# Optimization experiments

Measured on AMD Instinct MI355X. Metric: run time of the kernel, lower is better.

## Reference

```python
import jax, jax.numpy as jnp
import numpy as np

B, S, I, H, A = 512, 256, 12, 256, 9


def _lstm_layer(x, w_ih, w_hh, b_ih, b_hh):
    # x: [B,S,in] -> outputs [B,S,H], final (h, c). PyTorch gate order i,f,g,o.
    b, s, _ = x.shape
    h_dim = w_hh.shape[1]
    xg = jnp.einsum('bsi,gi->bsg', x, w_ih) + b_ih  # [B,S,4H] precomputed input gates

    def step(carry, xg_t):
        h, c = carry
        gates = xg_t + h @ w_hh.T + b_hh
        i_g, f_g, g_g, o_g = jnp.split(gates, 4, axis=-1)
        c = jax.nn.sigmoid(f_g) * c + jax.nn.sigmoid(i_g) * jnp.tanh(g_g)
        h = jax.nn.sigmoid(o_g) * jnp.tanh(c)
        return (h, c), h

    init = (jnp.zeros((b, h_dim), x.dtype), jnp.zeros((b, h_dim), x.dtype))
    (h, c), ys = jax.lax.scan(step, init, jnp.swapaxes(xg, 0, 1))
    return jnp.swapaxes(ys, 0, 1), h, c


def setup_inputs() -> dict:
    key = jax.random.key(0)
    ks = jax.random.split(key, 20)
    sc = 0.1
    inp = {
        'x': jax.random.normal(ks[0], (B, S, I), jnp.float32),
        'mask': jnp.ones((B, A), jnp.float32),
        'W_emb': jax.random.normal(ks[1], (H, I), jnp.float32) * sc,
        'b_emb': jnp.zeros((H,), jnp.float32),
        'w_ih0': jax.random.normal(ks[2], (4 * H, H), jnp.float32) * sc,
        'w_hh0': jax.random.normal(ks[3], (4 * H, H), jnp.float32) * sc,
        'b_ih0': jnp.zeros((4 * H,), jnp.float32),
        'b_hh0': jnp.zeros((4 * H,), jnp.float32),
        'w_ih1': jax.random.normal(ks[4], (4 * H, H), jnp.float32) * sc,
        'w_hh1': jax.random.normal(ks[5], (4 * H, H), jnp.float32) * sc,
        'b_ih1': jnp.zeros((4 * H,), jnp.float32),
        'b_hh1': jnp.zeros((4 * H,), jnp.float32),
        'ln_g': jnp.ones((H,), jnp.float32),
        'ln_b': jnp.zeros((H,), jnp.float32),
        'w1': jax.random.normal(ks[6], (32, H), jnp.float32) * sc,
        'b1': jnp.zeros((32,), jnp.float32),
        'w2': jax.random.normal(ks[7], (A, 32), jnp.float32) * sc,
        'b2': jnp.zeros((A,), jnp.float32),
    }
    return inp


def reference(x, mask, W_emb, b_emb, w_ih0, w_hh0, b_ih0, b_hh0,
              w_ih1, w_hh1, b_ih1, b_hh1, ln_g, ln_b, w1, b1, w2, b2):
    # embed + ReLU
    emb = jax.nn.relu(jnp.einsum('bsi,hi->bsh', x, W_emb) + b_emb)  # [B,S,H]
    # 2-layer LSTM (dropout between layers is identity in eval mode)
    y0, h0, c0 = _lstm_layer(emb, w_ih0, w_hh0, b_ih0, b_hh0)
    y1, h1, c1 = _lstm_layer(y0, w_ih1, w_hh1, b_ih1, b_hh1)
    last = y1[:, -1, :]  # [B,H]
    # LayerNorm
    mu = jnp.mean(last, axis=-1, keepdims=True)
    var = jnp.mean((last - mu) ** 2, axis=-1, keepdims=True)
    normed = (last - mu) / jnp.sqrt(var + 1e-5) * ln_g + ln_b
    # MLP head (dropout identity in eval)
    hdn = jax.nn.relu(normed @ w1.T + b1)
    logits = hdn @ w2.T + b2  # [B,A]
    logits = logits + (1.0 - mask) * -1e9
    hidden = (jnp.stack([h0, h1]), jnp.stack([c0, c1]))
    return logits, hidden
```

## Files before the change

### kernel.cpp

```cpp
#include <hip/hip_runtime.h>
#include <cstdint>
#include <cstddef>

typedef __attribute__((ext_vector_type(8))) short short8;
typedef __attribute__((ext_vector_type(4))) float f32x4;

#define MFMA16(a, b, c) __builtin_amdgcn_mfma_f32_16x16x32_bf16((a), (b), (c), 0, 0, 0)

constexpr int kB = 512, kS = 256, kI = 12, kH = 256, kA = 9;
constexpr int kNS = 8;
constexpr int kNB = 32;
constexpr int LDH = 264;
constexpr int LDG = 132;
constexpr int kBH = kB * kH;

constexpr int OUT_H = kB * kA;
constexpr int OUT_C = OUT_H + 2 * kB * kH;

__device__ __forceinline__ short f2bf(float f) {
  uint32_t u = __float_as_uint(f);
  u += 0x7fffu + ((u >> 16) & 1u);
  return (short)(u >> 16);
}
__device__ __forceinline__ float fast_sigmoid(float v) {
  return __builtin_amdgcn_rcpf(1.f + __expf(-v));
}
__device__ __forceinline__ float fast_tanh(float v) {
  return 2.f * __builtin_amdgcn_rcpf(1.f + __expf(-2.f * v)) - 1.f;
}

__global__ __launch_bounds__(256, 1) void lstm_scan_kernel(
    const float* __restrict__ x,
    const float* __restrict__ W_emb, const float* __restrict__ b_emb,
    const float* __restrict__ w_ih0, const float* __restrict__ w_hh0,
    const float* __restrict__ b_ih0, const float* __restrict__ b_hh0,
    const float* __restrict__ w_ih1, const float* __restrict__ w_hh1,
    const float* __restrict__ b_ih1, const float* __restrict__ b_hh1,
    unsigned short* __restrict__ h0ex, unsigned short* __restrict__ h1ex,
    int* __restrict__ flags0, int* __restrict__ flags1,
    float* __restrict__ dout)
{
  const int tid   = threadIdx.x;
  const int btile = blockIdx.x & (kNB - 1);
  const int slice = blockIdx.x >> 5;
  const int b0    = btile * 16;
  const int lane  = tid & 63;
  const int wave  = tid >> 6;
  const int n16   = lane & 15;
  const int quad  = lane >> 4;

  __shared__ short xlds[16 * 32];
  __shared__ short embL[16 * LDH];
  __shared__ short hA[16 * LDH];
  __shared__ short hB[16 * LDH];
  __shared__ float gL[16 * LDG];

  for (int i = tid; i < 16 * 32; i += 256) xlds[i] = 0;
  for (int i = tid; i < 16 * LDH; i += 256) { hA[i] = 0; hB[i] = 0; }

  const float* Wm[4] = { w_ih0, w_hh0, w_ih1, w_hh1 };
  short8 wB[2][4][8];
#pragma unroll
  for (int ti = 0; ti < 2; ++ti) {
    const int nt   = wave + ti * 4;
    const int gcol = (nt >> 1) * kH + slice * 32 + (nt & 1) * 16 + n16;
#pragma unroll
    for (int mat = 0; mat < 4; ++mat) {
      const float* wp = Wm[mat] + (size_t)gcol * kH;
#pragma unroll
      for (int kk = 0; kk < 8; ++kk) {
        const float* p = wp + kk * 32 + quad * 8;
        const float4 f0 = *(const float4*)p;
        const float4 f1 = *(const float4*)(p + 4);
        short8 v;
        v[0] = f2bf(f0.x); v[1] = f2bf(f0.y); v[2] = f2bf(f0.z); v[3] = f2bf(f0.w);
        v[4] = f2bf(f1.x); v[5] = f2bf(f1.y); v[6] = f2bf(f1.z); v[7] = f2bf(f1.w);
        wB[ti][mat][kk] = v;
      }
    }
  }
  short8 wE[4];
  float bembv[4];
#pragma unroll
  for (int i = 0; i < 4; ++i) {
    const int col = wave * 64 + i * 16 + n16;
    short8 v;
#pragma unroll
    for (int j = 0; j < 8; ++j) {
      const int k = quad * 8 + j;
      v[j] = (k < kI) ? f2bf(W_emb[col * kI + k]) : (short)0;
    }
    wE[i] = v;
    bembv[i] = b_emb[col];
  }
  const int m_ew = tid & 15;
  const int p2   = (tid >> 4) * 2;
  float bi0[2][4], bi1[2][4];
#pragma unroll
  for (int j = 0; j < 2; ++j) {
    const int col = slice * 32 + p2 + j;
#pragma unroll
    for (int g = 0; g < 4; ++g) {
      bi0[j][g] = b_ih0[g * kH + col] + b_hh0[g * kH + col];
      bi1[j][g] = b_ih1[g * kH + col] + b_hh1[g * kH + col];
    }
  }
  float c0v[2] = {0.f, 0.f}, c1v[2] = {0.f, 0.f};

  const int mr = tid / kI, kc = tid - (tid / kI) * kI;

  __syncthreads();

  if (tid < 192) xlds[mr * 32 + kc] = f2bf(x[((size_t)(b0 + mr) * kS + 0) * kI + kc]);
  __syncthreads();
  {
    const short8 xa = *(const short8*)&xlds[n16 * 32 + quad * 8];
#pragma unroll
    for (int i = 0; i < 4; ++i) {
      f32x4 z = {0.f, 0.f, 0.f, 0.f};
      f32x4 e = MFMA16(xa, wE[i], z);
      const int col = wave * 64 + i * 16 + n16;
#pragma unroll
      for (int r = 0; r < 4; ++r) {
        float v = e[r] + bembv[i];
        v = v > 0.f ? v : 0.f;
        embL[(quad * 4 + r) * LDH + col] = f2bf(v);
      }
    }
  }
  __syncthreads();

  int* const f0base = flags0 + (size_t)btile * kS;
  int* const f1base = flags1 + (size_t)btile * kS;

  for (int t = 0; t < kS; ++t) {
    float xreg = 0.f;
    if (t + 1 < kS && tid < 192)
      xreg = x[((size_t)(b0 + mr) * kS + (t + 1)) * kI + kc];

    {
      f32x4 acc0 = {0.f, 0.f, 0.f, 0.f}, acc1 = {0.f, 0.f, 0.f, 0.f};
#pragma unroll
      for (int kk = 0; kk < 8; ++kk) {
        const short8 a = *(const short8*)&embL[n16 * LDH + kk * 32 + quad * 8];
        acc0 = MFMA16(a, wB[0][0][kk], acc0);
        acc1 = MFMA16(a, wB[1][0][kk], acc1);
      }
#pragma unroll
      for (int kk = 0; kk < 8; ++kk) {
        const short8 a = *(const short8*)&hA[n16 * LDH + kk * 32 + quad * 8];
        acc0 = MFMA16(a, wB[0][1][kk], acc0);
        acc1 = MFMA16(a, wB[1][1][kk], acc1);
      }
#pragma unroll
      for (int ti = 0; ti < 2; ++ti) {
        const int nt = wave + ti * 4;
        const int lcol = (nt >> 1) * 32 + (nt & 1) * 16 + n16;
        const f32x4 a = ti ? acc1 : acc0;
#pragma unroll
        for (int r = 0; r < 4; ++r) gL[(quad * 4 + r) * LDG + lcol] = a[r];
      }
    }
    __syncthreads();

    {
      float hj[2];
#pragma unroll
      for (int j = 0; j < 2; ++j) {
        const int u = p2 + j;
        const float iv = gL[m_ew * LDG +       u] + bi0[j][0];
        const float fv = gL[m_ew * LDG +  32 + u] + bi0[j][1];
        const float gv = gL[m_ew * LDG +  64 + u] + bi0[j][2];
        const float ov = gL[m_ew * LDG +  96 + u] + bi0[j][3];
        const float c = fast_sigmoid(fv) * c0v[j] + fast_sigmoid(iv) * fast_tanh(gv);
        c0v[j] = c;
        hj[j] = fast_sigmoid(ov) * fast_tanh(c);
      }
      const uint32_t pk = (uint32_t)(uint16_t)f2bf(hj[0]) |
                          ((uint32_t)(uint16_t)f2bf(hj[1]) << 16);
      uint32_t* dst = (uint32_t*)&h0ex[(size_t)(t & 1) * kBH + (size_t)(b0 + m_ew) * kH + slice * 32 + p2];
      __hip_atomic_store(dst, pk, __ATOMIC_RELAXED, __HIP_MEMORY_SCOPE_AGENT);
      if (t == kS - 1) {
#pragma unroll
        for (int j = 0; j < 2; ++j) {
          const int col = slice * 32 + p2 + j;
          dout[OUT_H + (size_t)(b0 + m_ew) * kH + col] = hj[j];
          dout[OUT_C + (size_t)(b0 + m_ew) * kH + col] = c0v[j];
        }
      }
    }
    __syncthreads();

    if (tid == 0)
      __hip_atomic_fetch_add(f0base + t, 1, __ATOMIC_RELAXED, __HIP_MEMORY_SCOPE_AGENT);

    if (t + 1 < kS) {
      if (tid < 192) xlds[mr * 32 + kc] = f2bf(xreg);
      __syncthreads();
      const short8 xa = *(const short8*)&xlds[n16 * 32 + quad * 8];
#pragma unroll
      for (int i = 0; i < 4; ++i) {
        f32x4 z = {0.f, 0.f, 0.f, 0.f};
        f32x4 e = MFMA16(xa, wE[i], z);
        const int col = wave * 64 + i * 16 + n16;
#pragma unroll
        for (int r = 0; r < 4; ++r) {
          float v = e[r] + bembv[i];
          v = v > 0.f ? v : 0.f;
          embL[(quad * 4 + r) * LDH + col] = f2bf(v);
        }
      }
    }

    if (tid == 0) {
      while (__hip_atomic_load(f0base + t, __ATOMIC_RELAXED, __HIP_MEMORY_SCOPE_AGENT) < kNS)
        __builtin_amdgcn_s_sleep(1);
      if (t > 0)
        while (__hip_atomic_load(f1base + (t - 1), __ATOMIC_RELAXED, __HIP_MEMORY_SCOPE_AGENT) < kNS)
          __builtin_amdgcn_s_sleep(1);
    }
    __syncthreads();

    {
      const int rr = tid >> 4;
      const int cc = (tid & 15) * 16;
      const uint64_t* s0 = (const uint64_t*)&h0ex[(size_t)(t & 1) * kBH + (size_t)(b0 + rr) * kH + cc];
      uint64_t a0 = __hip_atomic_load(s0 + 0, __ATOMIC_RELAXED, __HIP_MEMORY_SCOPE_AGENT);
      uint64_t a1 = __hip_atomic_load(s0 + 1, __ATOMIC_RELAXED, __HIP_MEMORY_SCOPE_AGENT);
      uint64_t a2 = __hip_atomic_load(s0 + 2, __ATOMIC_RELAXED, __HIP_MEMORY_SCOPE_AGENT);
      uint64_t a3 = __hip_atomic_load(s0 + 3, __ATOMIC_RELAXED, __HIP_MEMORY_SCOPE_AGENT);
      uint64_t* dA = (uint64_t*)&hA[rr * LDH + cc];
      dA[0] = a0; dA[1] = a1; dA[2] = a2; dA[3] = a3;
      if (t > 0) {
        const uint64_t* s1 = (const uint64_t*)&h1ex[(size_t)((t - 1) & 1) * kBH + (size_t)(b0 + rr) * kH + cc];
        uint64_t b0v = __hip_atomic_load(s1 + 0, __ATOMIC_RELAXED, __HIP_MEMORY_SCOPE_AGENT);
        uint64_t b1v = __hip_atomic_load(s1 + 1, __ATOMIC_RELAXED, __HIP_MEMORY_SCOPE_AGENT);
        uint64_t b2v = __hip_atomic_load(s1 + 2, __ATOMIC_RELAXED, __HIP_MEMORY_SCOPE_AGENT);
        uint64_t b3v = __hip_atomic_load(s1 + 3, __ATOMIC_RELAXED, __HIP_MEMORY_SCOPE_AGENT);
        uint64_t* dB = (uint64_t*)&hB[rr * LDH + cc];
        dB[0] = b0v; dB[1] = b1v; dB[2] = b2v; dB[3] = b3v;
      }
    }
    __syncthreads();

    {
      f32x4 acc0 = {0.f, 0.f, 0.f, 0.f}, acc1 = {0.f, 0.f, 0.f, 0.f};
#pragma unroll
      for (int kk = 0; kk < 8; ++kk) {
        const short8 a = *(const short8*)&hA[n16 * LDH + kk * 32 + quad * 8];
        acc0 = MFMA16(a, wB[0][2][kk], acc0);
        acc1 = MFMA16(a, wB[1][2][kk], acc1);
      }
#pragma unroll
      for (int kk = 0; kk < 8; ++kk) {
        const short8 a = *(const short8*)&hB[n16 * LDH + kk * 32 + quad * 8];
        acc0 = MFMA16(a, wB[0][3][kk], acc0);
        acc1 = MFMA16(a, wB[1][3][kk], acc1);
      }
#pragma unroll
      for (int ti = 0; ti < 2; ++ti) {
        const int nt = wave + ti * 4;
        const int lcol = (nt >> 1) * 32 + (nt & 1) * 16 + n16;
        const f32x4 a = ti ? acc1 : acc0;
#pragma unroll
        for (int r = 0; r < 4; ++r) gL[(quad * 4 + r) * LDG + lcol] = a[r];
      }
    }
    __syncthreads();

    {
      float hj[2];
#pragma unroll
      for (int j = 0; j < 2; ++j) {
        const int u = p2 + j;
        const float iv = gL[m_ew * LDG +       u] + bi1[j][0];
        const float fv = gL[m_ew * LDG +  32 + u] + bi1[j][1];
        const float gv = gL[m_ew * LDG +  64 + u] + bi1[j][2];
        const float ov = gL[m_ew * LDG +  96 + u] + bi1[j][3];
        const float c = fast_sigmoid(fv) * c1v[j] + fast_sigmoid(iv) * fast_tanh(gv);
        c1v[j] = c;
        hj[j] = fast_sigmoid(ov) * fast_tanh(c);
      }
      const uint32_t pk = (uint32_t)(uint16_t)f2bf(hj[0]) |
                          ((uint32_t)(uint16_t)f2bf(hj[1]) << 16);
      uint32_t* dst = (uint32_t*)&h1ex[(size_t)(t & 1) * kBH + (size_t)(b0 + m_ew) * kH + slice * 32 + p2];
      __hip_atomic_store(dst, pk, __ATOMIC_RELAXED, __HIP_MEMORY_SCOPE_AGENT);
      if (t == kS - 1) {
#pragma unroll
        for (int j = 0; j < 2; ++j) {
          const int col = slice * 32 + p2 + j;
          dout[OUT_H + kBH + (size_t)(b0 + m_ew) * kH + col] = hj[j];
          dout[OUT_C + kBH + (size_t)(b0 + m_ew) * kH + col] = c1v[j];
        }
      }
    }
    __syncthreads();

    if (tid == 0)
      __hip_atomic_fetch_add(f1base + t, 1, __ATOMIC_RELAXED, __HIP_MEMORY_SCOPE_AGENT);
  }
}

__global__ __launch_bounds__(64) void head_kernel(
    const float* __restrict__ h1last, const float* __restrict__ mask,
    const float* __restrict__ ln_g, const float* __restrict__ ln_b,
    const float* __restrict__ w1, const float* __restrict__ b1,
    const float* __restrict__ w2, const float* __restrict__ b2,
    float* __restrict__ out)
{
  const int r = blockIdx.x;
  const int lane = threadIdx.x;
  __shared__ float ns[kH];
  __shared__ float hd[32];
  const float4 v = *(const float4*)&h1last[r * kH + lane * 4];
  float vv[4] = {v.x, v.y, v.z, v.w};
  float s = vv[0] + vv[1] + vv[2] + vv[3];
#pragma unroll
  for (int off = 32; off > 0; off >>= 1) s += __shfl_xor(s, off, 64);
  const float mean = s * (1.f / kH);
  float q = 0.f;
#pragma unroll
  for (int j = 0; j < 4; ++j) { const float d = vv[j] - mean; q += d * d; }
#pragma unroll
  for (int off = 32; off > 0; off >>= 1) q += __shfl_xor(q, off, 64);
  const float rstd = rsqrtf(q * (1.f / kH) + 1e-5f);
#pragma unroll
  for (int j = 0; j < 4; ++j) {
    const int c = lane * 4 + j;
    ns[c] = (vv[j] - mean) * rstd * ln_g[c] + ln_b[c];
  }
  __syncthreads();
  if (lane < 32) {
    float a = b1[lane];
    const float* wr = w1 + lane * kH;
    for (int k = 0; k < kH; ++k) a += ns[k] * wr[k];
    hd[lane] = a > 0.f ? a : 0.f;
  }
  __syncthreads();
  if (lane < kA) {
    float a = b2[lane];
    const float* wr = w2 + lane * 32;
#pragma unroll
    for (int k = 0; k < 32; ++k) a += hd[k] * wr[k];
    a += (1.f - mask[r * kA + lane]) * (-1e9f);
    out[r * kA + lane] = a;
  }
}

extern "C" void kernel_launch(void* const* d_in, const int* in_sizes, int n_in,
                              void* d_out, int out_size, void* d_ws, size_t ws_size,
                              hipStream_t stream)
{
  (void)in_sizes; (void)n_in; (void)out_size; (void)ws_size;
  const float* x     = (const float*)d_in[0];
  const float* mask  = (const float*)d_in[1];
  const float* W_emb = (const float*)d_in[2];
  const float* b_emb = (const float*)d_in[3];
  const float* w_ih0 = (const float*)d_in[4];
  const float* w_hh0 = (const float*)d_in[5];
  const float* b_ih0 = (const float*)d_in[6];
  const float* b_hh0 = (const float*)d_in[7];
  const float* w_ih1 = (const float*)d_in[8];
  const float* w_hh1 = (const float*)d_in[9];
  const float* b_ih1 = (const float*)d_in[10];
  const float* b_hh1 = (const float*)d_in[11];
  const float* ln_g  = (const float*)d_in[12];
  const float* ln_b  = (const float*)d_in[13];
  const float* w1    = (const float*)d_in[14];
  const float* b1    = (const float*)d_in[15];
  const float* w2    = (const float*)d_in[16];
  const float* b2    = (const float*)d_in[17];
  float* out = (float*)d_out;

  unsigned short* h0ex = (unsigned short*)d_ws;
  unsigned short* h1ex = h0ex + 2 * kBH;
  const size_t exch_bytes = (size_t)2 * (2 * kBH) * sizeof(unsigned short);
  int* flags0 = (int*)((char*)d_ws + exch_bytes);
  int* flags1 = flags0 + kNB * kS;
  const size_t flag_bytes = (size_t)2 * kNB * kS * sizeof(int);

  hipMemsetAsync(flags0, 0, flag_bytes, stream);

  lstm_scan_kernel<<<dim3(kNB * kNS), dim3(256), 0, stream>>>(
      x, W_emb, b_emb, w_ih0, w_hh0, b_ih0, b_hh0, w_ih1, w_hh1, b_ih1, b_hh1,
      h0ex, h1ex, flags0, flags1, out);

  head_kernel<<<dim3(kB), dim3(64), 0, stream>>>(
      out + OUT_H + kBH, mask, ln_g, ln_b, w1, b1, w2, b2, out);
}
```

Before: 1.157 ms.

## Wavefront-pipeline the two LSTM layers so each step needs one grid barrier

The two layers are now skewed by one timestep. In each pass layer 0 computes step p while layer 1 computes step p-1, both from the same exchanged hidden states, so one flag barrier and one exchange load replace the two per-step barriers. The x staging buffer in shared memory is removed: lanes now read x straight into MFMA operand registers. This halves the cross-block synchronisations along the serial critical path. In exchange it adds an extra pass, a zero-initialised h1 exchange buffer, and more MFMA work per pass.

```diff
diff --git a/kernel.cpp b/kernel.cpp
--- a/kernel.cpp
+++ b/kernel.cpp
@@ -13,9 +13,10 @@
 constexpr int LDH = 264;
 constexpr int LDG = 132;
 constexpr int kBH = kB * kH;
+constexpr int FLS = 512;
 
 constexpr int OUT_H = kB * kA;
-constexpr int OUT_C = OUT_H + 2 * kB * kH;
+constexpr int OUT_C = OUT_H + 2 * kBH;
 
 __device__ __forceinline__ short f2bf(float f) {
   uint32_t u = __float_as_uint(f);
@@ -37,7 +38,7 @@
     const float* __restrict__ w_ih1, const float* __restrict__ w_hh1,
     const float* __restrict__ b_ih1, const float* __restrict__ b_hh1,
     unsigned short* __restrict__ h0ex, unsigned short* __restrict__ h1ex,
-    int* __restrict__ flags0, int* __restrict__ flags1,
+    int* __restrict__ flags,
     float* __restrict__ dout)
 {
   const int tid   = threadIdx.x;
@@ -49,13 +50,12 @@
   const int n16   = lane & 15;
   const int quad  = lane >> 4;
 
-  __shared__ short xlds[16 * 32];
   __shared__ short embL[16 * LDH];
   __shared__ short hA[16 * LDH];
   __shared__ short hB[16 * LDH];
-  __shared__ float gL[16 * LDG];
-
-  for (int i = tid; i < 16 * 32; i += 256) xlds[i] = 0;
+  __shared__ float gL0[16 * LDG];
+  __shared__ float gL1[16 * LDG];
+
   for (int i = tid; i < 16 * LDH; i += 256) { hA[i] = 0; hB[i] = 0; }
 
   const float* Wm[4] = { w_ih0, w_hh0, w_ih1, w_hh1 };
@@ -93,12 +93,12 @@
     wE[i] = v;
     bembv[i] = b_emb[col];
   }
-  const int m_ew = tid & 15;
-  const int p2   = (tid >> 4) * 2;
+  const int erow = tid >> 4;
+  const int ec   = (tid & 15) * 2;
   float bi0[2][4], bi1[2][4];
 #pragma unroll
   for (int j = 0; j < 2; ++j) {
-    const int col = slice * 32 + p2 + j;
+    const int col = slice * 32 + ec + j;
 #pragma unroll
     for (int g = 0; g < 4; ++g) {
       bi0[j][g] = b_ih0[g * kH + col] + b_hh0[g * kH + col];
@@ -107,14 +107,14 @@
   }
   float c0v[2] = {0.f, 0.f}, c1v[2] = {0.f, 0.f};
 
-  const int mr = tid / kI, kc = tid - (tid / kI) * kI;
-
-  __syncthreads();
-
-  if (tid < 192) xlds[mr * 32 + kc] = f2bf(x[((size_t)(b0 + mr) * kS + 0) * kI + kc]);
-  __syncthreads();
   {
-    const short8 xa = *(const short8*)&xlds[n16 * 32 + quad * 8];
+    const float* xr = x + (size_t)(b0 + n16) * kS * kI;
+    short8 xa;
+#pragma unroll
+    for (int j = 0; j < 8; ++j) {
+      const int k = quad * 8 + j;
+      xa[j] = (k < kI) ? f2bf(xr[k]) : (short)0;
+    }
 #pragma unroll
     for (int i = 0; i < 4; ++i) {
       f32x4 z = {0.f, 0.f, 0.f, 0.f};
@@ -130,174 +130,152 @@
   }
   __syncthreads();
 
-  int* const f0base = flags0 + (size_t)btile * kS;
-  int* const f1base = flags1 + (size_t)btile * kS;
-
-  for (int t = 0; t < kS; ++t) {
-    float xreg = 0.f;
-    if (t + 1 < kS && tid < 192)
-      xreg = x[((size_t)(b0 + mr) * kS + (t + 1)) * kI + kc];
+  int* const fl = flags + btile * FLS;
+
+  for (int p = 0; p <= kS; ++p) {
+    const int par = p & 1;
 
     {
-      f32x4 acc0 = {0.f, 0.f, 0.f, 0.f}, acc1 = {0.f, 0.f, 0.f, 0.f};
+      f32x4 a0 = {0.f,0.f,0.f,0.f}, a1 = a0, g1b0 = a0, g1b1 = a0;
 #pragma unroll
       for (int kk = 0; kk < 8; ++kk) {
-        const short8 a = *(const short8*)&embL[n16 * LDH + kk * 32 + quad * 8];
-        acc0 = MFMA16(a, wB[0][0][kk], acc0);
-        acc1 = MFMA16(a, wB[1][0][kk], acc1);
+        const short8 ha = *(const short8*)&hA[n16 * LDH + kk * 32 + quad * 8];
+        a0   = MFMA16(ha, wB[0][1][kk], a0);
+        a1   = MFMA16(ha, wB[1][1][kk], a1);
+        g1b0 = MFMA16(ha, wB[0][2][kk], g1b0);
+        g1b1 = MFMA16(ha, wB[1][2][kk], g1b1);
       }
 #pragma unroll
       for (int kk = 0; kk < 8; ++kk) {
-        const short8 a = *(const short8*)&hA[n16 * LDH + kk * 32 + quad * 8];
-        acc0 = MFMA16(a, wB[0][1][kk], acc0);
-        acc1 = MFMA16(a, wB[1][1][kk], acc1);
+        const short8 e = *(const short8*)&embL[n16 * LDH + kk * 32 + quad * 8];
+        a0 = MFMA16(e, wB[0][0][kk], a0);
+        a1 = MFMA16(e, wB[1][0][kk], a1);
+      }
+#pragma unroll
+      for (int kk = 0; kk < 8; ++kk) {
+        const short8 hb = *(const short8*)&hB[n16 * LDH + kk * 32 + quad * 8];
+        g1b0 = MFMA16(hb, wB[0][3][kk], g1b0);
+        g1b1 = MFMA16(hb, wB[1][3][kk], g1b1);
       }
 #pragma unroll
       for (int ti = 0; ti < 2; ++ti) {
         const int nt = wave + ti * 4;
         const int lcol = (nt >> 1) * 32 + (nt & 1) * 16 + n16;
-        const f32x4 a = ti ? acc1 : acc0;
-#pragma unroll
-        for (int r = 0; r < 4; ++r) gL[(quad * 4 + r) * LDG + lcol] = a[r];
+        const f32x4 va = ti ? a1 : a0;
+        const f32x4 vb = ti ? g1b1 : g1b0;
+#pragma unroll
+        for (int r = 0; r < 4; ++r) {
+          gL0[(quad * 4 + r) * LDG + lcol] = va[r];
+          gL1[(quad * 4 + r) * LDG + lcol] = vb[r];
+        }
       }
     }
     __syncthreads();
 
-    {
+    if (p < kS) {
       float hj[2];
 #pragma unroll
       for (int j = 0; j < 2; ++j) {
-        const int u = p2 + j;
-        const float iv = gL[m_ew * LDG +       u] + bi0[j][0];
-        const float fv = gL[m_ew * LDG +  32 + u] + bi0[j][1];
-        const float gv = gL[m_ew * LDG +  64 + u] + bi0[j][2];
-        const float ov = gL[m_ew * LDG +  96 + u] + bi0[j][3];
+        const int u = ec + j;
+        const float iv = gL0[erow * LDG +       u] + bi0[j][0];
+        const float fv = gL0[erow * LDG +  32 + u] + bi0[j][1];
+        const float gv = gL0[erow * LDG +  64 + u] + bi0[j][2];
+        const float ov = gL0[erow * LDG +  96 + u] + bi0[j][3];
         const float c = fast_sigmoid(fv) * c0v[j] + fast_sigmoid(iv) * fast_tanh(gv);
         c0v[j] = c;
         hj[j] = fast_sigmoid(ov) * fast_tanh(c);
       }
       const uint32_t pk = (uint32_t)(uint16_t)f2bf(hj[0]) |
                           ((uint32_t)(uint16_t)f2bf(hj[1]) << 16);
-      uint32_t* dst = (uint32_t*)&h0ex[(size_t)(t & 1) * kBH + (size_t)(b0 + m_ew) * kH + slice * 32 + p2];
+      uint32_t* dst = (uint32_t*)&h0ex[(size_t)par * kBH + (size_t)(b0 + erow) * kH + slice * 32 + ec];
       __hip_atomic_store(dst, pk, __ATOMIC_RELAXED, __HIP_MEMORY_SCOPE_AGENT);
-      if (t == kS - 1) {
+      if (p == kS - 1) {
 #pragma unroll
         for (int j = 0; j < 2; ++j) {
-          const int col = slice * 32 + p2 + j;
-          dout[OUT_H + (size_t)(b0 + m_ew) * kH + col] = hj[j];
-          dout[OUT_C + (size_t)(b0 + m_ew) * kH + col] = c0v[j];
-        }
-      }
-    }
-    __syncthreads();
-
-    if (tid == 0)
-      __hip_atomic_fetch_add(f0base + t, 1, __ATOMIC_RELAXED, __HIP_MEMORY_SCOPE_AGENT);
-
-    if (t + 1 < kS) {
-      if (tid < 192) xlds[mr * 32 + kc] = f2bf(xreg);
-      __syncthreads();
-      const short8 xa = *(const short8*)&xlds[n16 * 32 + quad * 8];
-#pragma unroll
-      for (int i = 0; i < 4; ++i) {
-        f32x4 z = {0.f, 0.f, 0.f, 0.f};
-        f32x4 e = MFMA16(xa, wE[i], z);
-        const int col = wave * 64 + i * 16 + n16;
-#pragma unroll
-        for (int r = 0; r < 4; ++r) {
-          float v = e[r] + bembv[i];
-          v = v > 0.f ? v : 0.f;
-          embL[(quad * 4 + r) * LDH + col] = f2bf(v);
-        }
-      }
-    }
-
-    if (tid == 0) {
-      while (__hip_atomic_load(f0base + t, __ATOMIC_RELAXED, __HIP_MEMORY_SCOPE_AGENT) < kNS)
-        __builtin_amdgcn_s_sleep(1);
-      if (t > 0)
-        while (__hip_atomic_load(f1base + (t - 1), __ATOMIC_RELAXED, __HIP_MEMORY_SCOPE_AGENT) < kNS)
-          __builtin_amdgcn_s_sleep(1);
-    }
-    __syncthreads();
-
-    {
-      const int rr = tid >> 4;
-      const int cc = (tid & 15) * 16;
-      const uint64_t* s0 = (const uint64_t*)&h0ex[(size_t)(t & 1) * kBH + (size_t)(b0 + rr) * kH + cc];
-      uint64_t a0 = __hip_atomic_load(s0 + 0, __ATOMIC_RELAXED, __HIP_MEMORY_SCOPE_AGENT);
-      uint64_t a1 = __hip_atomic_load(s0 + 1, __ATOMIC_RELAXED, __HIP_MEMORY_SCOPE_AGENT);
-      uint64_t a2 = __hip_atomic_load(s0 + 2, __ATOMIC_RELAXED, __HIP_MEMORY_SCOPE_AGENT);
-      uint64_t a3 = __hip_atomic_load(s0 + 3, __ATOMIC_RELAXED, __HIP_MEMORY_SCOPE_AGENT);
-      uint64_t* dA = (uint64_t*)&hA[rr * LDH + cc];
-      dA[0] = a0; dA[1] = a1; dA[2] = a2; dA[3] = a3;
-      if (t > 0) {
-        const uint64_t* s1 = (const uint64_t*)&h1ex[(size_t)((t - 1) & 1) * kBH + (size_t)(b0 + rr) * kH + cc];
-        uint64_t b0v = __hip_atomic_load(s1 + 0, __ATOMIC_RELAXED, __HIP_MEMORY_SCOPE_AGENT);
-        uint64_t b1v = __hip_atomic_load(s1 + 1, __ATOMIC_RELAXED, __HIP_MEMORY_SCOPE_AGENT);
-        uint64_t b2v = __hip_atomic_load(s1 + 2, __ATOMIC_RELAXED, __HIP_MEMORY_SCOPE_AGENT);
-        uint64_t b3v = __hip_atomic_load(s1 + 3, __ATOMIC_RELAXED, __HIP_MEMORY_SCOPE_AGENT);
-        uint64_t* dB = (uint64_t*)&hB[rr * LDH + cc];
-        dB[0] = b0v; dB[1] = b1v; dB[2] = b2v; dB[3] = b3v;
-      }
-    }
-    __syncthreads();
-
-    {
-      f32x4 acc0 = {0.f, 0.f, 0.f, 0.f}, acc1 = {0.f, 0.f, 0.f, 0.f};
-#pragma unroll
-      for (int kk = 0; kk < 8; ++kk) {
-        const short8 a = *(const short8*)&hA[n16 * LDH + kk * 32 + quad * 8];
-        acc0 = MFMA16(a, wB[0][2][kk], acc0);
-        acc1 = MFMA16(a, wB[1][2][kk], acc1);
-      }
-#pragma unroll
-      for (int kk = 0; kk < 8; ++kk) {
-        const short8 a = *(const short8*)&hB[n16 * LDH + kk * 32 + quad * 8];
-        acc0 = MFMA16(a, wB[0][3][kk], acc0);
-        acc1 = MFMA16(a, wB[1][3][kk], acc1);
-      }
-#pragma unroll
-      for (int ti = 0; ti < 2; ++ti) {
-        const int nt = wave + ti * 4;
-        const int lcol = (nt >> 1) * 32 + (nt & 1) * 16 + n16;
-        const f32x4 a = ti ? acc1 : acc0;
-#pragma unroll
-        for (int r = 0; r < 4; ++r) gL[(quad * 4 + r) * LDG + lcol] = a[r];
-      }
-    }
-    __syncthreads();
-
-    {
+          const int col = slice * 32 + ec + j;
+          dout[OUT_H + (size_t)(b0 + erow) * kH + col] = hj[j];
+          dout[OUT_C + (size_t)(b0 + erow) * kH + col] = c0v[j];
+        }
+      }
+    }
+    if (p >= 1) {
       float hj[2];
 #pragma unroll
       for (int j = 0; j < 2; ++j) {
-        const int u = p2 + j;
-        const float iv = gL[m_ew * LDG +       u] + bi1[j][0];
-        const float fv = gL[m_ew * LDG +  32 + u] + bi1[j][1];
-        const float gv = gL[m_ew * LDG +  64 + u] + bi1[j][2];
-        const float ov = gL[m_ew * LDG +  96 + u] + bi1[j][3];
+        const int u = ec + j;
+        const float iv = gL1[erow * LDG +       u] + bi1[j][0];
+        const float fv = gL1[erow * LDG +  32 + u] + bi1[j][1];
+        const float gv = gL1[erow * LDG +  64 + u] + bi1[j][2];
+        const float ov = gL1[erow * LDG +  96 + u] + bi1[j][3];
         const float c = fast_sigmoid(fv) * c1v[j] + fast_sigmoid(iv) * fast_tanh(gv);
         c1v[j] = c;
         hj[j] = fast_sigmoid(ov) * fast_tanh(c);
       }
       const uint32_t pk = (uint32_t)(uint16_t)f2bf(hj[0]) |
                           ((uint32_t)(uint16_t)f2bf(hj[1]) << 16);
-      uint32_t* dst = (uint32_t*)&h1ex[(size_t)(t & 1) * kBH + (size_t)(b0 + m_ew) * kH + slice * 32 + p2];
+      uint32_t* dst = (uint32_t*)&h1ex[(size_t)par * kBH + (size_t)(b0 + erow) * kH + slice * 32 + ec];
       __hip_atomic_store(dst, pk, __ATOMIC_RELAXED, __HIP_MEMORY_SCOPE_AGENT);
-      if (t == kS - 1) {
+      if (p == kS) {
 #pragma unroll
         for (int j = 0; j < 2; ++j) {
-          const int col = slice * 32 + p2 + j;
-          dout[OUT_H + kBH + (size_t)(b0 + m_ew) * kH + col] = hj[j];
-          dout[OUT_C + kBH + (size_t)(b0 + m_ew) * kH + col] = c1v[j];
+          const int col = slice * 32 + ec + j;
+          dout[OUT_H + kBH + (size_t)(b0 + erow) * kH + col] = hj[j];
+          dout[OUT_C + kBH + (size_t)(b0 + erow) * kH + col] = c1v[j];
         }
       }
     }
     __syncthreads();
 
-    if (tid == 0)
-      __hip_atomic_fetch_add(f1base + t, 1, __ATOMIC_RELAXED, __HIP_MEMORY_SCOPE_AGENT);
+    if (p < kS) {
+      if (tid == 0)
+        __hip_atomic_fetch_add(fl + p, 1, __ATOMIC_RELAXED, __HIP_MEMORY_SCOPE_AGENT);
+
+      if (p + 1 < kS) {
+        const float* xr = x + ((size_t)(b0 + n16) * kS + (p + 1)) * kI;
+        short8 xa;
+#pragma unroll
+        for (int j = 0; j < 8; ++j) {
+          const int k = quad * 8 + j;
+          xa[j] = (k < kI) ? f2bf(xr[k]) : (short)0;
+        }
+#pragma unroll
+        for (int i = 0; i < 4; ++i) {
+          f32x4 z = {0.f, 0.f, 0.f, 0.f};
+          f32x4 e = MFMA16(xa, wE[i], z);
+          const int col = wave * 64 + i * 16 + n16;
+#pragma unroll
+          for (int r = 0; r < 4; ++r) {
+            float v = e[r] + bembv[i];
+            v = v > 0.f ? v : 0.f;
+            embL[(quad * 4 + r) * LDH + col] = f2bf(v);
+          }
+        }
+      }
+
+      while (__hip_atomic_load(fl + p, __ATOMIC_RELAXED, __HIP_MEMORY_SCOPE_AGENT) < kNS)
+        __builtin_amdgcn_s_sleep(1);
+
+      {
+        const int rr = tid >> 4;
+        const int cc = (tid & 15) * 16;
+        const size_t base = (size_t)par * kBH + (size_t)(b0 + rr) * kH + cc;
+        const uint64_t* s0 = (const uint64_t*)&h0ex[base];
+        const uint64_t* s1 = (const uint64_t*)&h1ex[base];
+        uint64_t va0 = __hip_atomic_load(s0 + 0, __ATOMIC_RELAXED, __HIP_MEMORY_SCOPE_AGENT);
+        uint64_t va1 = __hip_atomic_load(s0 + 1, __ATOMIC_RELAXED, __HIP_MEMORY_SCOPE_AGENT);
+        uint64_t va2 = __hip_atomic_load(s0 + 2, __ATOMIC_RELAXED, __HIP_MEMORY_SCOPE_AGENT);
+        uint64_t va3 = __hip_atomic_load(s0 + 3, __ATOMIC_RELAXED, __HIP_MEMORY_SCOPE_AGENT);
+        uint64_t vb0 = __hip_atomic_load(s1 + 0, __ATOMIC_RELAXED, __HIP_MEMORY_SCOPE_AGENT);
+        uint64_t vb1 = __hip_atomic_load(s1 + 1, __ATOMIC_RELAXED, __HIP_MEMORY_SCOPE_AGENT);
+        uint64_t vb2 = __hip_atomic_load(s1 + 2, __ATOMIC_RELAXED, __HIP_MEMORY_SCOPE_AGENT);
+        uint64_t vb3 = __hip_atomic_load(s1 + 3, __ATOMIC_RELAXED, __HIP_MEMORY_SCOPE_AGENT);
+        uint64_t* dA = (uint64_t*)&hA[rr * LDH + cc];
+        uint64_t* dB = (uint64_t*)&hB[rr * LDH + cc];
+        dA[0] = va0; dA[1] = va1; dA[2] = va2; dA[3] = va3;
+        dB[0] = vb0; dB[1] = vb1; dB[2] = vb2; dB[3] = vb3;
+      }
+      __syncthreads();
+    }
   }
 }
 
@@ -374,16 +352,15 @@
 
   unsigned short* h0ex = (unsigned short*)d_ws;
   unsigned short* h1ex = h0ex + 2 * kBH;
-  const size_t exch_bytes = (size_t)2 * (2 * kBH) * sizeof(unsigned short);
-  int* flags0 = (int*)((char*)d_ws + exch_bytes);
-  int* flags1 = flags0 + kNB * kS;
-  const size_t flag_bytes = (size_t)2 * kNB * kS * sizeof(int);
-
-  hipMemsetAsync(flags0, 0, flag_bytes, stream);
+  int* flags = (int*)(h1ex + 2 * kBH);
+  const size_t flag_bytes = (size_t)kNB * FLS * sizeof(int);
+
+  hipMemsetAsync(flags, 0, flag_bytes, stream);
+  hipMemsetAsync(h1ex, 0, (size_t)kBH * sizeof(unsigned short), stream);
 
   lstm_scan_kernel<<<dim3(kNB * kNS), dim3(256), 0, stream>>>(
       x, W_emb, b_emb, w_ih0, w_hh0, b_ih0, b_hh0, w_ih1, w_hh1, b_ih1, b_hh1,
-      h0ex, h1ex, flags0, flags1, out);
+      h0ex, h1ex, flags, out);
 
   head_kernel<<<dim3(kB), dim3(64), 0, stream>>>(
       out + OUT_H + kBH, mask, ln_g, ln_b, w1, b1, w2, b2, out);
```

After: 1.173 ms. No clear change (+1.4%).
